# Kernel tuning notes

Hardware: AMD Instinct MI355X
Metric: run time of the kernel (lower is better)

## Reference

```python
import jax, jax.numpy as jnp
import numpy as np

B, C, F_IN, F_OUT = 4096, 63, 250, 250
NEG_SLOPE = 0.2  # GATConv default negative_slope


def setup_inputs() -> dict:
    key = jax.random.key(0)
    ks = jax.random.split(key, 5)
    return {
        "x": jax.random.normal(ks[0], (B, 1, C, F_IN), dtype=jnp.float32),
        "W": jax.random.normal(ks[1], (F_IN, F_OUT), dtype=jnp.float32) / np.sqrt(F_IN),
        "att_src": jax.random.normal(ks[2], (F_OUT,), dtype=jnp.float32) / np.sqrt(F_OUT),
        "att_dst": jax.random.normal(ks[3], (F_OUT,), dtype=jnp.float32) / np.sqrt(F_OUT),
        "bias": jax.random.normal(ks[4], (F_OUT,), dtype=jnp.float32) * 0.01,
    }


def reference(x, W, att_src, att_dst, bias):
    # x: [B, 1, C, F_in] -> per-batch graph of C=63 nodes, fully connected
    # (all i!=j edges plus GATConv's default self-loops => dense C x C attention).
    h = jnp.einsum("bcf,fo->bco", x[:, 0], W)          # [B, C, F_out] node embeddings
    a_s = jnp.einsum("bco,o->bc", h, att_src)           # per-source score
    a_d = jnp.einsum("bco,o->bc", h, att_dst)           # per-destination score
    # e[b, dst, src] = leakyrelu(a_s[src] + a_d[dst]); softmax over sources per dst
    e = jax.nn.leaky_relu(a_s[:, None, :] + a_d[:, :, None], NEG_SLOPE)  # [B, C, C]
    alpha = jax.nn.softmax(e, axis=-1)
    out = jnp.einsum("bds,bso->bdo", alpha, h) + bias   # [B, C, F_out]
    return out[:, None]                                  # [B, 1, C, F_out]
```

## Files before the change

kernel.cpp:

```cpp
#include <hip/hip_runtime.h>
#include <hip/hip_bf16.h>

typedef __bf16 bf16;
typedef __attribute__((ext_vector_type(8))) __bf16 bf16x8;
typedef __attribute__((ext_vector_type(4))) __bf16 bf16x4;
typedef __attribute__((ext_vector_type(2))) __bf16 bf16x2;
typedef __attribute__((ext_vector_type(4))) float f32x4;

#define C_NODES 63
#define F_DIM   250
#define NEG_SLOPE 0.2f

#define OFF_AS    32000
#define OFF_AD    32256
#define OFF_ALPHA 32768
#define LDS_BYTES 40960

__device__ __forceinline__ int swz(int a) { return a ^ ((a >> 3) & 0x70); }

extern "C" __global__ __launch_bounds__(256)
void gat_prep(const float* __restrict__ W, const float* __restrict__ att_src,
              const float* __restrict__ att_dst, bf16* __restrict__ Wp) {
    int i = blockIdx.x * 256 + threadIdx.x;
    int tile = i >> 9;
    int ln   = (i >> 3) & 63;
    int j    = i & 7;
    int kt = tile >> 4, nt = tile & 15;
    int k = kt * 32 + (ln >> 4) * 8 + j;
    int n = nt * 16 + (ln & 15);
    float v = 0.f;
    if (k < F_DIM) {
        if (n < F_DIM) {
            v = W[k * F_DIM + n];
        } else if (n == F_DIM || n == F_DIM + 1) {
            const float* att = (n == F_DIM) ? att_src : att_dst;
            float s = 0.f;
            for (int o = 0; o < F_DIM; ++o) s = fmaf(W[k * F_DIM + o], att[o], s);
            v = s;
        }
    }
    Wp[i] = (bf16)v;
}

extern "C" __global__ __launch_bounds__(256, 4)
void gat_main(const float* __restrict__ x, const bf16* __restrict__ Wp,
              const float* __restrict__ bias, float* __restrict__ out)
{
    __shared__ __align__(16) unsigned char smem[LDS_BYTES];
    const int tid  = threadIdx.x;
    const int lane = tid & 63;
    const int w    = tid >> 6;
    const int b    = blockIdx.x;
    const int fl   = lane & 15;
    const int fh   = lane >> 4;

    float bv[4];
#pragma unroll
    for (int nti = 0; nti < 4; ++nti) {
        int f = w * 64 + nti * 16 + fl;
        bv[nti] = (f < F_DIM) ? bias[f] : 0.f;
    }

    if (tid < 64) {
        int base = (((tid >> 4) * 8 + 7) << 10) + (48 + (tid & 15)) * 16;
        *(unsigned int*)(smem + base + 4) = 0u;
        *(unsigned long long*)(smem + base + 8) = 0ull;
    } else if (tid < 96) {
        int idx = tid - 64;
        int base = ((24 + (idx >> 2)) << 10) + ((((idx & 3) << 4) | 15) * 16);
        *(f32x4*)(smem + base) = (f32x4){0.f, 0.f, 0.f, 0.f};
    }

    {
        const float* xb = x + (size_t)b * (C_NODES * F_DIM);
#pragma unroll
        for (int it = 0; it < 8; ++it) {
            int idx = tid + it * 256;
            if (idx < 2016) {
                int r = idx >> 5, g = idx & 31;
                const float* src = xb + r * F_DIM + g * 8;
                int dl = (r & 15) | ((g & 3) << 4);
                int base = (((r >> 4) * 8 + (g >> 2)) << 10) + dl * 16;
                if (g < 31) {
                    float2 v0 = *(const float2*)(src);
                    float2 v1 = *(const float2*)(src + 2);
                    float2 v2 = *(const float2*)(src + 4);
                    float2 v3 = *(const float2*)(src + 6);
                    bf16x8 pk = { (bf16)v0.x, (bf16)v0.y, (bf16)v1.x, (bf16)v1.y,
                                  (bf16)v2.x, (bf16)v2.y, (bf16)v3.x, (bf16)v3.y };
                    *(bf16x8*)(smem + base) = pk;
                } else {
                    float2 v0 = *(const float2*)(src);
                    bf16x2 pk = { (bf16)v0.x, (bf16)v0.y };
                    *(bf16x2*)(smem + base) = pk;
                }
            }
        }
    }
    __syncthreads();

    f32x4 acc[4][4];
#pragma unroll
    for (int mt = 0; mt < 4; ++mt)
#pragma unroll
        for (int nti = 0; nti < 4; ++nti)
            acc[mt][nti] = (f32x4){0.f, 0.f, 0.f, 0.f};
    {
        const bf16x8* afrv = (const bf16x8*)(smem);
        const bf16x8* wpv  = (const bf16x8*)Wp;
#pragma unroll 2
        for (int kt = 0; kt < 8; ++kt) {
            bf16x8 af[4], bw[4];
#pragma unroll
            for (int mt = 0; mt < 4; ++mt)
                af[mt] = afrv[(mt * 8 + kt) * 64 + lane];
#pragma unroll
            for (int nti = 0; nti < 4; ++nti)
                bw[nti] = wpv[(kt * 16 + (w * 4 + nti)) * 64 + lane];
#pragma unroll
            for (int mt = 0; mt < 4; ++mt)
#pragma unroll
                for (int nti = 0; nti < 4; ++nti)
                    acc[mt][nti] = __builtin_amdgcn_mfma_f32_16x16x32_bf16(
                        af[mt], bw[nti], acc[mt][nti], 0, 0, 0);
        }
    }
    __syncthreads();

    {
#pragma unroll
        for (int mt = 0; mt < 4; ++mt) {
            int s0 = mt * 16 + fh * 4;
#pragma unroll
            for (int nti = 0; nti < 4; ++nti) {
                int f = w * 64 + nti * 16 + fl;
                if (f < F_DIM) {
                    f32x4 v = acc[mt][nti];
                    bf16x4 hv = { (bf16)v.x, (bf16)v.y, (bf16)v.z, (bf16)v.w };
                    *(bf16x4*)(smem + swz(f * 128 + s0 * 2)) = hv;
                }
            }
        }
        if (w == 3 && (fl == 10 || fl == 11)) {
            float* dst = (float*)(smem + (fl == 10 ? OFF_AS : OFF_AD));
#pragma unroll
            for (int mt = 0; mt < 4; ++mt) {
                f32x4 v = acc[mt][3];
#pragma unroll
                for (int i = 0; i < 4; ++i) dst[mt * 16 + fh * 4 + i] = v[i];
            }
        }
    }
    __syncthreads();

    {
        const float* AS  = (const float*)(smem + OFF_AS);
        const float* ADp = (const float*)(smem + OFF_AD);
        int d  = tid >> 2;
        int sq = tid & 3;
        float ad_v = ADp[d];
        f32x4 a0 = *(const f32x4*)(AS + sq * 16);
        f32x4 a1 = *(const f32x4*)(AS + sq * 16 + 4);
        f32x4 a2 = *(const f32x4*)(AS + sq * 16 + 8);
        f32x4 a3 = *(const f32x4*)(AS + sq * 16 + 12);
        float le[16];
#pragma unroll
        for (int k = 0; k < 4; ++k) {
            float e;
            e = a0[k] + ad_v; le[k]      = (e > 0.f) ? e : NEG_SLOPE * e;
            e = a1[k] + ad_v; le[4 + k]  = (e > 0.f) ? e : NEG_SLOPE * e;
            e = a2[k] + ad_v; le[8 + k]  = (e > 0.f) ? e : NEG_SLOPE * e;
            e = a3[k] + ad_v; le[12 + k] = (e > 0.f) ? e : NEG_SLOPE * e;
        }
        if (sq == 3) le[15] = -3.0e38f;
        float md = le[0];
#pragma unroll
        for (int k = 1; k < 16; ++k) md = fmaxf(md, le[k]);
        md = fmaxf(md, __shfl_xor(md, 1));
        md = fmaxf(md, __shfl_xor(md, 2));
        float p[16], sum = 0.f;
#pragma unroll
        for (int k = 0; k < 16; ++k) { p[k] = __expf(le[k] - md); sum += p[k]; }
        sum += __shfl_xor(sum, 1);
        sum += __shfl_xor(sum, 2);
        float rz = 1.f / sum;
        bf16x8 pk0, pk1;
#pragma unroll
        for (int k = 0; k < 8; ++k) {
            pk0[k] = (bf16)(p[k] * rz);
            pk1[k] = (bf16)(p[8 + k] * rz);
        }
        int base = OFF_ALPHA + d * 128 + sq * 32;
        *(bf16x8*)(smem + swz(base))      = pk0;
        *(bf16x8*)(smem + swz(base + 16)) = pk1;
    }
    __syncthreads();

    f32x4 acc2[4][4];
#pragma unroll
    for (int mt = 0; mt < 4; ++mt)
#pragma unroll
        for (int nti = 0; nti < 4; ++nti)
            acc2[mt][nti] = (f32x4){0.f, 0.f, 0.f, 0.f};
    {
#pragma unroll
        for (int ks = 0; ks < 2; ++ks) {
            int kk = ks * 32 + fh * 8;
            bf16x8 aal[4], hbf[4];
#pragma unroll
            for (int mt = 0; mt < 4; ++mt) {
                int dd = mt * 16 + fl;
                aal[mt] = *(const bf16x8*)(smem + swz(OFF_ALPHA + dd * 128 + kk * 2));
            }
#pragma unroll
            for (int nti = 0; nti < 4; ++nti) {
                int f = w * 64 + nti * 16 + fl;
                hbf[nti] = *(const bf16x8*)(smem + swz(f * 128 + kk * 2));
            }
#pragma unroll
            for (int mt = 0; mt < 4; ++mt)
#pragma unroll
                for (int nti = 0; nti < 4; ++nti)
                    acc2[mt][nti] = __builtin_amdgcn_mfma_f32_16x16x32_bf16(
                        aal[mt], hbf[nti], acc2[mt][nti], 0, 0, 0);
        }
    }

    float* ob = out + (size_t)b * (C_NODES * F_DIM);
#pragma unroll
    for (int mt = 0; mt < 4; ++mt) {
#pragma unroll
        for (int i = 0; i < 4; ++i) {
            int r = mt * 16 + fh * 4 + i;
            if (r < C_NODES) {
#pragma unroll
                for (int nti = 0; nti < 4; ++nti) {
                    int f = w * 64 + nti * 16 + fl;
                    if (f < F_DIM) ob[r * F_DIM + f] = acc2[mt][nti][i] + bv[nti];
                }
            }
        }
    }
}

extern "C" void kernel_launch(void* const* d_in, const int* in_sizes, int n_in,
                              void* d_out, int out_size, void* d_ws, size_t ws_size,
                              hipStream_t stream) {
    const float* x       = (const float*)d_in[0];
    const float* W       = (const float*)d_in[1];
    const float* att_src = (const float*)d_in[2];
    const float* att_dst = (const float*)d_in[3];
    const float* bias    = (const float*)d_in[4];
    float* out = (float*)d_out;
    bf16* Wp = (bf16*)d_ws;

    gat_prep<<<256, 256, 0, stream>>>(W, att_src, att_dst, Wp);
    gat_main<<<4096, 256, 0, stream>>>(x, Wp, bias, out);
}
```

Before: 147.6 us.

## Compute softmax alpha in MFMA fragment layout in registers, swizzle x LDS tile

Each wave now computes the attention softmax directly in the A-fragment layout the second MFMA needs, keeping alpha in registers. This removes the LDS alpha buffer, a barrier and the alpha LDS reads, and shrinks LDS to 32KB. The x tile in LDS gets an XOR swizzle to reduce bank conflicts, and the first two W k-tiles are prefetched from global before the x load, with the GEMM loop fully unrolled. The cost is that each wave recomputes the full 63x63 softmax redundantly (four times across the block) and register pressure rises, which may hurt occupancy under the 4-block launch bound.

Measured after the change: 185.7 us. 25.8% more time.

```diff
diff --git a/kernel.cpp b/kernel.cpp
--- a/kernel.cpp
+++ b/kernel.cpp
@@ -13,10 +13,12 @@
 
 #define OFF_AS    32000
 #define OFF_AD    32256
-#define OFF_ALPHA 32768
-#define LDS_BYTES 40960
+#define LDS_BYTES 32768
 
 __device__ __forceinline__ int swz(int a) { return a ^ ((a >> 3) & 0x70); }
+__device__ __forceinline__ int swzA(int a) {
+    return a ^ ((((a >> 8) & 3) ^ ((a >> 10) & 3)) << 4) ^ (((a >> 12) & 1) << 6);
+}
 
 extern "C" __global__ __launch_bounds__(256)
 void gat_prep(const float* __restrict__ W, const float* __restrict__ att_src,
@@ -54,6 +56,16 @@
     const int fl   = lane & 15;
     const int fh   = lane >> 4;
 
+    const bf16x8* wpv = (const bf16x8*)Wp;
+
+    bf16x8 bwpre0[4], bwpre1[4];
+#pragma unroll
+    for (int nti = 0; nti < 4; ++nti)
+        bwpre0[nti] = wpv[(w * 4 + nti) * 64 + lane];
+#pragma unroll
+    for (int nti = 0; nti < 4; ++nti)
+        bwpre1[nti] = wpv[(16 + w * 4 + nti) * 64 + lane];
+
     float bv[4];
 #pragma unroll
     for (int nti = 0; nti < 4; ++nti) {
@@ -62,12 +74,12 @@
     }
 
     if (tid < 64) {
-        int base = (((tid >> 4) * 8 + 7) << 10) + (48 + (tid & 15)) * 16;
+        int base = swzA((((tid >> 4) * 8 + 7) << 10) + (48 + (tid & 15)) * 16);
         *(unsigned int*)(smem + base + 4) = 0u;
         *(unsigned long long*)(smem + base + 8) = 0ull;
     } else if (tid < 96) {
         int idx = tid - 64;
-        int base = ((24 + (idx >> 2)) << 10) + ((((idx & 3) << 4) | 15) * 16);
+        int base = swzA(((24 + (idx >> 2)) << 10) + ((((idx & 3) << 4) | 15) * 16));
         *(f32x4*)(smem + base) = (f32x4){0.f, 0.f, 0.f, 0.f};
     }
 
@@ -80,7 +92,7 @@
                 int r = idx >> 5, g = idx & 31;
                 const float* src = xb + r * F_DIM + g * 8;
                 int dl = (r & 15) | ((g & 3) << 4);
-                int base = (((r >> 4) * 8 + (g >> 2)) << 10) + dl * 16;
+                int base = swzA((((r >> 4) * 8 + (g >> 2)) << 10) + dl * 16);
                 if (g < 31) {
                     float2 v0 = *(const float2*)(src);
                     float2 v1 = *(const float2*)(src + 2);
@@ -105,25 +117,23 @@
 #pragma unroll
         for (int nti = 0; nti < 4; ++nti)
             acc[mt][nti] = (f32x4){0.f, 0.f, 0.f, 0.f};
-    {
-        const bf16x8* afrv = (const bf16x8*)(smem);
-        const bf16x8* wpv  = (const bf16x8*)Wp;
-#pragma unroll 2
-        for (int kt = 0; kt < 8; ++kt) {
-            bf16x8 af[4], bw[4];
-#pragma unroll
-            for (int mt = 0; mt < 4; ++mt)
-                af[mt] = afrv[(mt * 8 + kt) * 64 + lane];
+#pragma unroll
+    for (int kt = 0; kt < 8; ++kt) {
+        bf16x8 af[4], bw[4];
+#pragma unroll
+        for (int nti = 0; nti < 4; ++nti)
+            bw[nti] = (kt == 0) ? bwpre0[nti]
+                    : (kt == 1) ? bwpre1[nti]
+                    : wpv[(kt * 16 + (w * 4 + nti)) * 64 + lane];
+#pragma unroll
+        for (int mt = 0; mt < 4; ++mt)
+            af[mt] = *(const bf16x8*)(smem + swzA(((mt * 8 + kt) << 10) + lane * 16));
+#pragma unroll
+        for (int mt = 0; mt < 4; ++mt)
 #pragma unroll
             for (int nti = 0; nti < 4; ++nti)
-                bw[nti] = wpv[(kt * 16 + (w * 4 + nti)) * 64 + lane];
-#pragma unroll
-            for (int mt = 0; mt < 4; ++mt)
-#pragma unroll
-                for (int nti = 0; nti < 4; ++nti)
-                    acc[mt][nti] = __builtin_amdgcn_mfma_f32_16x16x32_bf16(
-                        af[mt], bw[nti], acc[mt][nti], 0, 0, 0);
-        }
+                acc[mt][nti] = __builtin_amdgcn_mfma_f32_16x16x32_bf16(
+                    af[mt], bw[nti], acc[mt][nti], 0, 0, 0);
     }
     __syncthreads();
 
@@ -153,48 +163,48 @@
     }
     __syncthreads();
 
+    bf16x8 aal[4][2];
     {
         const float* AS  = (const float*)(smem + OFF_AS);
         const float* ADp = (const float*)(smem + OFF_AD);
-        int d  = tid >> 2;
-        int sq = tid & 3;
-        float ad_v = ADp[d];
-        f32x4 a0 = *(const f32x4*)(AS + sq * 16);
-        f32x4 a1 = *(const f32x4*)(AS + sq * 16 + 4);
-        f32x4 a2 = *(const f32x4*)(AS + sq * 16 + 8);
-        f32x4 a3 = *(const f32x4*)(AS + sq * 16 + 12);
-        float le[16];
-#pragma unroll
-        for (int k = 0; k < 4; ++k) {
-            float e;
-            e = a0[k] + ad_v; le[k]      = (e > 0.f) ? e : NEG_SLOPE * e;
-            e = a1[k] + ad_v; le[4 + k]  = (e > 0.f) ? e : NEG_SLOPE * e;
-            e = a2[k] + ad_v; le[8 + k]  = (e > 0.f) ? e : NEG_SLOPE * e;
-            e = a3[k] + ad_v; le[12 + k] = (e > 0.f) ? e : NEG_SLOPE * e;
-        }
-        if (sq == 3) le[15] = -3.0e38f;
-        float md = le[0];
-#pragma unroll
-        for (int k = 1; k < 16; ++k) md = fmaxf(md, le[k]);
-        md = fmaxf(md, __shfl_xor(md, 1));
-        md = fmaxf(md, __shfl_xor(md, 2));
-        float p[16], sum = 0.f;
-#pragma unroll
-        for (int k = 0; k < 16; ++k) { p[k] = __expf(le[k] - md); sum += p[k]; }
-        sum += __shfl_xor(sum, 1);
-        sum += __shfl_xor(sum, 2);
-        float rz = 1.f / sum;
-        bf16x8 pk0, pk1;
-#pragma unroll
-        for (int k = 0; k < 8; ++k) {
-            pk0[k] = (bf16)(p[k] * rz);
-            pk1[k] = (bf16)(p[8 + k] * rz);
-        }
-        int base = OFF_ALPHA + d * 128 + sq * 32;
-        *(bf16x8*)(smem + swz(base))      = pk0;
-        *(bf16x8*)(smem + swz(base + 16)) = pk1;
-    }
-    __syncthreads();
+        f32x4 s0 = *(const f32x4*)(AS + fh * 8);
+        f32x4 s1 = *(const f32x4*)(AS + fh * 8 + 4);
+        f32x4 s2 = *(const f32x4*)(AS + 32 + fh * 8);
+        f32x4 s3 = *(const f32x4*)(AS + 32 + fh * 8 + 4);
+#pragma unroll
+        for (int mt = 0; mt < 4; ++mt) {
+            float ad_v = ADp[mt * 16 + fl];
+            float le[16];
+#pragma unroll
+            for (int k = 0; k < 4; ++k) {
+                float e;
+                e = s0[k] + ad_v; le[k]      = (e > 0.f) ? e : NEG_SLOPE * e;
+                e = s1[k] + ad_v; le[4 + k]  = (e > 0.f) ? e : NEG_SLOPE * e;
+                e = s2[k] + ad_v; le[8 + k]  = (e > 0.f) ? e : NEG_SLOPE * e;
+                e = s3[k] + ad_v; le[12 + k] = (e > 0.f) ? e : NEG_SLOPE * e;
+            }
+            if (fh == 3) le[15] = -3.0e38f;
+            float md = le[0];
+#pragma unroll
+            for (int k = 1; k < 16; ++k) md = fmaxf(md, le[k]);
+            md = fmaxf(md, __shfl_xor(md, 16));
+            md = fmaxf(md, __shfl_xor(md, 32));
+            float p[16], sum = 0.f;
+#pragma unroll
+            for (int k = 0; k < 16; ++k) { p[k] = __expf(le[k] - md); sum += p[k]; }
+            sum += __shfl_xor(sum, 16);
+            sum += __shfl_xor(sum, 32);
+            float rz = 1.f / sum;
+            bf16x8 a0, a1;
+#pragma unroll
+            for (int k = 0; k < 8; ++k) {
+                a0[k] = (bf16)(p[k] * rz);
+                a1[k] = (bf16)(p[8 + k] * rz);
+            }
+            aal[mt][0] = a0;
+            aal[mt][1] = a1;
+        }
+    }
 
     f32x4 acc2[4][4];
 #pragma unroll
@@ -202,28 +212,21 @@
 #pragma unroll
         for (int nti = 0; nti < 4; ++nti)
             acc2[mt][nti] = (f32x4){0.f, 0.f, 0.f, 0.f};
-    {
-#pragma unroll
-        for (int ks = 0; ks < 2; ++ks) {
-            int kk = ks * 32 + fh * 8;
-            bf16x8 aal[4], hbf[4];
-#pragma unroll
-            for (int mt = 0; mt < 4; ++mt) {
-                int dd = mt * 16 + fl;
-                aal[mt] = *(const bf16x8*)(smem + swz(OFF_ALPHA + dd * 128 + kk * 2));
-            }
-#pragma unroll
-            for (int nti = 0; nti < 4; ++nti) {
-                int f = w * 64 + nti * 16 + fl;
-                hbf[nti] = *(const bf16x8*)(smem + swz(f * 128 + kk * 2));
-            }
-#pragma unroll
-            for (int mt = 0; mt < 4; ++mt)
-#pragma unroll
-                for (int nti = 0; nti < 4; ++nti)
-                    acc2[mt][nti] = __builtin_amdgcn_mfma_f32_16x16x32_bf16(
-                        aal[mt], hbf[nti], acc2[mt][nti], 0, 0, 0);
-        }
+#pragma unroll
+    for (int ks = 0; ks < 2; ++ks) {
+        int kk = ks * 32 + fh * 8;
+        bf16x8 hbf[4];
+#pragma unroll
+        for (int nti = 0; nti < 4; ++nti) {
+            int f = w * 64 + nti * 16 + fl;
+            hbf[nti] = *(const bf16x8*)(smem + swz(f * 128 + kk * 2));
+        }
+#pragma unroll
+        for (int mt = 0; mt < 4; ++mt)
+#pragma unroll
+            for (int nti = 0; nti < 4; ++nti)
+                acc2[mt][nti] = __builtin_amdgcn_mfma_f32_16x16x32_bf16(
+                    aal[mt][ks], hbf[nti], acc2[mt][nti], 0, 0, 0);
     }
 
     float* ob = out + (size_t)b * (C_NODES * F_DIM);
```
